# Kernel tuning notes

Hardware: AMD Instinct MI355X
Metric: run time of the kernel (lower is better)

Reference implementation:

```python
import jax, jax.numpy as jnp
import numpy as np

EMBED_DIM = 2048
N_HEADS = 16
N_KV_HEADS = 4
HEAD_DIM = EMBED_DIM // N_HEADS  # 128
B, T = 8, 512


def _rope_tables(seq, dim):
    # matches RoPE.__init__: freqs repeated twice along last dim
    inv_freq = 1.0 / (10000.0 ** (jnp.arange(0, dim, 2, dtype=jnp.float32) / dim))
    t = jnp.arange(seq, dtype=jnp.float32)
    freqs = jnp.outer(t, inv_freq)          # [T, dim/2]
    emb = jnp.concatenate([freqs, freqs], axis=-1)  # [T, dim]
    return jnp.cos(emb), jnp.sin(emb)


def _apply_rope(x, cos, sin):
    # x: [B, H, T, D]; rotate-half convention
    d2 = x.shape[-1] // 2
    x1, x2 = x[..., :d2], x[..., d2:]
    x_rot = jnp.concatenate([-x2, x1], axis=-1)
    return x * cos[None, None] + x_rot * sin[None, None]


def setup_inputs() -> dict:
    key = jax.random.key(0)
    k1, k2, k3, k4, k5 = jax.random.split(key, 5)
    x = jax.random.normal(k1, (B, T, EMBED_DIM), dtype=jnp.float32)
    s = 1.0 / np.sqrt(EMBED_DIM)
    # weights stored [in, out] for y = x @ W
    wq = jax.random.normal(k2, (EMBED_DIM, EMBED_DIM), dtype=jnp.float32) * s
    wk = jax.random.normal(k3, (EMBED_DIM, HEAD_DIM * N_KV_HEADS), dtype=jnp.float32) * s
    wv = jax.random.normal(k4, (EMBED_DIM, HEAD_DIM * N_KV_HEADS), dtype=jnp.float32) * s
    wo = jax.random.normal(k5, (EMBED_DIM, EMBED_DIM), dtype=jnp.float32) * s
    # causal mask: 1 where attendable, 0 -> masked to -inf
    mask = jnp.tril(jnp.ones((T, T), dtype=bool))[None, None]  # [1,1,T,T]
    return {"x": x, "wq": wq, "wk": wk, "wv": wv, "wo": wo, "mask": mask}


def reference(x, wq, wk, wv, wo, mask):
    Bx, Tx, C = x.shape
    rep = N_HEADS // N_KV_HEADS
    q = (x @ wq).reshape(Bx, Tx, N_HEADS, HEAD_DIM).transpose(0, 2, 1, 3)      # [B,H,T,D]
    k = (x @ wk).reshape(Bx, Tx, N_KV_HEADS, HEAD_DIM).transpose(0, 2, 1, 3)   # [B,Hk,T,D]
    v = (x @ wv).reshape(Bx, Tx, N_KV_HEADS, HEAD_DIM).transpose(0, 2, 1, 3)
    cos, sin = _rope_tables(Tx, HEAD_DIM)
    q = _apply_rope(q, cos, sin)
    k = _apply_rope(k, cos, sin)
    k = jnp.repeat(k, rep, axis=1)  # GQA expand -> [B,H,T,D]
    v = jnp.repeat(v, rep, axis=1)
    scale = HEAD_DIM ** -0.5
    attn = jnp.einsum('bhtd,bhsd->bhts', q, k) * scale  # [B,H,T,T]
    attn = jnp.where(mask, attn, -jnp.inf)
    attn = jax.nn.softmax(attn, axis=-1)
    out = jnp.einsum('bhts,bhsd->bhtd', attn, v)        # [B,H,T,D]
    out = out.transpose(0, 2, 1, 3).reshape(Bx, Tx, C)
    return out @ wo
```

## Files before the change

kernel.cpp:

```cpp
#include <hip/hip_runtime.h>
#include <hip/hip_bf16.h>
#include <stdint.h>


typedef __bf16 bf16x8 __attribute__((ext_vector_type(8)));
typedef float  f32x4  __attribute__((ext_vector_type(4)));
typedef float  f4     __attribute__((ext_vector_type(4)));
typedef unsigned short u16x8 __attribute__((ext_vector_type(8)));
typedef unsigned short u16x4 __attribute__((ext_vector_type(4)));
typedef unsigned short us;

template<int V> struct Ic { static constexpr int v = V; };

__device__ __forceinline__ float bf2f(us u) {
  unsigned int x = ((unsigned int)u) << 16;
  return __builtin_bit_cast(float, x);
}
__device__ __forceinline__ us f2bf(float f) {
  unsigned int x = __builtin_bit_cast(unsigned int, f);
  unsigned int r = x + 0x7fffu + ((x >> 16) & 1u);
  return (us)(r >> 16);
}

__device__ __forceinline__ void gload16(const void* gsrc, void* ldst) {
  auto g = (const __attribute__((address_space(1))) void*)gsrc;
  auto l = (__attribute__((address_space(3))) void*)ldst;
  __builtin_amdgcn_global_load_lds(g, l, 16, 0, 0);
}

#define BAR() __builtin_amdgcn_s_barrier()
#define LGK0() do { asm volatile("s_waitcnt lgkmcnt(0)" ::: "memory"); \
                    __builtin_amdgcn_sched_barrier(0); } while (0)
#define VM0() do { asm volatile("s_waitcnt vmcnt(0)" ::: "memory"); \
                   __builtin_amdgcn_sched_barrier(0); } while (0)


__global__ void convx_kernel(const float* __restrict__ x, us* __restrict__ xb) {
  size_t idx = (size_t)blockIdx.x * 256 + threadIdx.x;
  const f4* p = (const f4*)(x + idx * 8);
  f4 a = p[0], b = p[1];
  u16x8 o;
#pragma unroll
  for (int e = 0; e < 4; ++e) { o[e] = f2bf(a[e]); o[4 + e] = f2bf(b[e]); }
  *(u16x8*)(xb + idx * 8) = o;
}

__global__ __launch_bounds__(256) void wtrans_kernel(const float* __restrict__ src,
    us* __restrict__ dst, int N, int rowOff, int LD) {
  __shared__ float lds[64][65];
  const int n0 = blockIdx.x * 64, k0 = blockIdx.y * 64;
  const int c = threadIdx.x & 63, rq = threadIdx.x >> 6;
#pragma unroll
  for (int i = 0; i < 16; ++i) {
    int r = i * 4 + rq;
    lds[r][c] = src[(size_t)(k0 + r) * N + n0 + c];
  }
  __syncthreads();
#pragma unroll
  for (int i = 0; i < 16; ++i) {
    int nr = i * 4 + rq;
    dst[(size_t)(rowOff + n0 + nr) * LD + k0 + c] = f2bf(lds[c][nr]);
  }
}

__global__ void tables_kernel(float* __restrict__ ct, float* __restrict__ st) {
  int idx = blockIdx.x * 256 + threadIdx.x;
  int i = idx & 63, t = idx >> 6;
  float inv = exp2f(-(float)i * (13.287712379549449f / 64.0f));
  float ang = (float)t * inv;
  ct[idx] = cosf(ang);
  st[idx] = sinf(ang);
}

__global__ void rope_kernel(us* __restrict__ Qh, us* __restrict__ Kh,
                            const float* __restrict__ ct, const float* __restrict__ st) {
  int idx = blockIdx.x * 256 + threadIdx.x;
  int dq = idx & 15;
  int t = (idx >> 4) & 511;
  int slot = idx >> 13;
  bool isQ = slot < 128;
  us* rowp = isQ ? (Qh + ((size_t)slot * 512 + t) * 128)
                 : (Kh + ((size_t)(slot - 128) * 512 + t) * 128);
  int d0 = dq * 4;
  u16x4 x1 = *(const u16x4*)(rowp + d0);
  u16x4 x2 = *(const u16x4*)(rowp + 64 + d0);
  f4 c = *(const f4*)(ct + t * 64 + d0);
  f4 s = *(const f4*)(st + t * 64 + d0);
  float scale = isQ ? 0.08838834764831845f : 1.0f;
  u16x4 o1, o2;
#pragma unroll
  for (int e = 0; e < 4; ++e) {
    float a = bf2f(x1[e]), b = bf2f(x2[e]);
    o1[e] = f2bf((a * c[e] - b * s[e]) * scale);
    o2[e] = f2bf((b * c[e] + a * s[e]) * scale);
  }
  *(u16x4*)(rowp + d0) = o1;
  *(u16x4*)(rowp + 64 + d0) = o2;
}

__global__ __launch_bounds__(256) void vtrans_kernel(const us* __restrict__ Vh,
                                                     us* __restrict__ Vt) {
  __shared__ us lds[64][66];
  const int bid = blockIdx.x;
  const int bhk = bid >> 4;
  const int rem = bid & 15;
  const int tt = rem >> 1, dt = rem & 1;
  const us* src = Vh + (size_t)bhk * 512 * 128;
  us* dst = Vt + (size_t)bhk * 128 * 512;
  const int c = threadIdx.x & 63, rq = threadIdx.x >> 6;
#pragma unroll
  for (int i = 0; i < 16; ++i) {
    int r = i * 4 + rq;
    lds[r][c] = src[(size_t)(tt * 64 + r) * 128 + dt * 64 + c];
  }
  __syncthreads();
#pragma unroll
  for (int i = 0; i < 16; ++i) {
    int dr = i * 4 + rq;
    dst[(size_t)(dt * 64 + dr) * 512 + tt * 64 + c] = lds[c][dr];
  }
}

template<int BM, int BN, int MF, int NF, int GPT, int WN>
__device__ __forceinline__ void gemm8_core(const us* __restrict__ A,
    const us* __restrict__ Bt, int K, int m0, int n0, us* sm,
    f32x4 (&acc)[MF][NF]) {
  constexpr int MH = MF / 2, NH = NF / 2;
  constexpr int ACH = BM * 8, CH2 = (BM + BN) * 4;
  constexpr int BBASE = 2 * BM * 64;
  const int tid = threadIdx.x, lane = tid & 63, wid = tid >> 6;
  const int wm = wid / WN, wn = wid % WN;
  const int lr = lane & 15, lq = lane >> 4;
  const int NT2 = K >> 7;

  const f32x4 zz = {0.f, 0.f, 0.f, 0.f};
#pragma unroll
  for (int i = 0; i < MF; ++i)
#pragma unroll
    for (int j = 0; j < NF; ++j) acc[i][j] = zz;

  bf16x8 afr[MH][2], bfr[NH][2];

  auto stage_half = [&](int kt, int hf) {
    const int q = kt & 1;
#pragma unroll
    for (int i = 0; i < GPT; ++i) {
      int c = hf * CH2 + i * 512 + tid;
      bool isA = (c < ACH);
      int cc = isA ? c : c - ACH;
      int row = cc >> 3;
      int kcs = (cc & 7) ^ (row & 7);
      const us* src = (isA ? A + (size_t)(m0 + row) * K
                           : Bt + (size_t)(n0 + row) * K) + (kt << 6) + (kcs << 3);
      us* dst = sm + (isA ? q * BM * 64 + cc * 8 : BBASE + q * BN * 64 + cc * 8);
      gload16(src, dst);
    }
  };
  auto lda = [&](int q, int mq) {
#pragma unroll
    for (int f = 0; f < MH; ++f) {
      int R = wm * (MF * 16) + mq * (MH * 16) + f * 16 + lr;
      int base = (q * BM * 64 + R * 64) * 2;
      int sw = (R & 7) << 4;
#pragma unroll
      for (int ks = 0; ks < 2; ++ks)
        afr[f][ks] = *(const bf16x8*)((const char*)sm + base + ((ks * 64 + lq * 16) ^ sw));
    }
  };
  auto ldb = [&](int q, int nq) {
#pragma unroll
    for (int g = 0; g < NH; ++g) {
      int R = wn * (NF * 16) + nq * (NH * 16) + g * 16 + lr;
      int base = (BBASE + q * BN * 64 + R * 64) * 2;
      int sw = (R & 7) << 4;
#pragma unroll
      for (int ks = 0; ks < 2; ++ks)
        bfr[g][ks] = *(const bf16x8*)((const char*)sm + base + ((ks * 64 + lq * 16) ^ sw));
    }
  };
  auto mmac = [&](auto MQ, auto NQ) {
    constexpr int mq = decltype(MQ)::v, nq = decltype(NQ)::v;
    __builtin_amdgcn_s_setprio(1);
#pragma unroll
    for (int ks = 0; ks < 2; ++ks)
#pragma unroll
      for (int f = 0; f < MH; ++f)
#pragma unroll
        for (int g = 0; g < NH; ++g)
          acc[mq * MH + f][nq * NH + g] = __builtin_amdgcn_mfma_f32_16x16x32_bf16(
              afr[f][ks], bfr[g][ks], acc[mq * MH + f][nq * NH + g], 0, 0, 0);
    __builtin_amdgcn_s_setprio(0);
  };

  stage_half(0, 0); stage_half(0, 1);
  VM0(); BAR();

  for (int it = 0; it < NT2; ++it) {
    const int k0 = 2 * it;
    const bool pf = (it + 1 < NT2);
    lda(0, 0); ldb(0, 0);
    stage_half(k0 + 1, 0);
    BAR(); LGK0(); mmac(Ic<0>{}, Ic<0>{}); BAR();

    ldb(0, 1);
    stage_half(k0 + 1, 1);
    BAR(); LGK0(); mmac(Ic<0>{}, Ic<1>{}); BAR();

    lda(0, 1);
    BAR(); LGK0(); mmac(Ic<1>{}, Ic<1>{}); BAR();

    ldb(0, 0);
    BAR(); LGK0(); mmac(Ic<1>{}, Ic<0>{});
    VM0();
    BAR();
    lda(1, 0); ldb(1, 0);
    if (pf) stage_half(k0 + 2, 0);
    BAR(); LGK0(); mmac(Ic<0>{}, Ic<0>{}); BAR();

    ldb(1, 1);
    if (pf) stage_half(k0 + 2, 1);
    BAR(); LGK0(); mmac(Ic<0>{}, Ic<1>{}); BAR();

    lda(1, 1);
    BAR(); LGK0(); mmac(Ic<1>{}, Ic<1>{}); BAR();

    ldb(1, 0);
    BAR(); LGK0(); mmac(Ic<1>{}, Ic<0>{});
    VM0();
    BAR();
  }
}

__global__ __launch_bounds__(512, 2) void gemm_qkv8_kernel(const us* __restrict__ xb,
    const us* __restrict__ wcat, us* __restrict__ Qh, us* __restrict__ Kh,
    us* __restrict__ Vh) {
  __shared__ __align__(16) us sm[65536];
  const int bid = blockIdx.x;
  const int swz = (bid & 7) * 24 + (bid >> 3);
  const int m0 = (swz & 15) << 8, n0 = (swz >> 4) << 8;
  f32x4 acc[8][4];
  gemm8_core<256, 256, 8, 4, 4, 4>(xb, wcat, 2048, m0, n0, sm, acc);

  const int tid = threadIdx.x, lane = tid & 63, wid = tid >> 6;
  const int wm = wid >> 2, wn = wid & 3, lr = lane & 15, lq = lane >> 4;
#pragma unroll
  for (int f = 0; f < 8; ++f)
#pragma unroll
    for (int g = 0; g < 4; ++g) {
      int col = n0 + wn * 64 + g * 16 + lr;
#pragma unroll
      for (int r = 0; r < 4; ++r) {
        int row = m0 + wm * 128 + f * 16 + lq * 4 + r;
        int bb = row >> 9, t = row & 511;
        us val = f2bf(acc[f][g][r]);
        if (col < 2048) {
          Qh[((size_t)(bb * 16 + (col >> 7)) * 512 + t) * 128 + (col & 127)] = val;
        } else if (col < 2560) {
          int cc = col - 2048;
          Kh[((size_t)(bb * 4 + (cc >> 7)) * 512 + t) * 128 + (cc & 127)] = val;
        } else {
          int cc = col - 2560;
          Vh[((size_t)(bb * 4 + (cc >> 7)) * 512 + t) * 128 + (cc & 127)] = val;
        }
      }
    }
}

__global__ __launch_bounds__(512, 2) void gemm_out8_kernel(const us* __restrict__ Ob,
    const us* __restrict__ wot, float* __restrict__ out) {
  __shared__ __align__(16) us sm[49152];
  const int bid = blockIdx.x;
  const int swz = (bid & 7) * 32 + (bid >> 3);
  const int m0 = (swz & 15) << 8, n0 = (swz >> 4) << 7;
  f32x4 acc[4][4];
  gemm8_core<256, 128, 4, 4, 3, 2>(Ob, wot, 2048, m0, n0, sm, acc);

  const int tid = threadIdx.x, lane = tid & 63, wid = tid >> 6;
  const int wm = wid >> 1, wn = wid & 1, lr = lane & 15, lq = lane >> 4;
#pragma unroll
  for (int f = 0; f < 4; ++f)
#pragma unroll
    for (int g = 0; g < 4; ++g) {
      int col = n0 + wn * 64 + g * 16 + lr;
#pragma unroll
      for (int r = 0; r < 4; ++r) {
        int row = m0 + wm * 64 + f * 16 + lq * 4 + r;
        out[(size_t)row * 2048 + col] = acc[f][g][r];
      }
    }
}

__global__ __launch_bounds__(256) void attn_kernel(const us* __restrict__ Qh,
    const us* __restrict__ Kh, const us* __restrict__ Vt, us* __restrict__ Oh) {
  __shared__ __align__(16) us Ktile[64 * 128];
  __shared__ __align__(16) us Vtile[128 * 64];
  __shared__ __align__(16) us Plds[4 * 16 * 72];
  const int tid = threadIdx.x, lane = tid & 63, w = tid >> 6;
  const int lr = lane & 15, lq = lane >> 4;
  const int qb = blockIdx.x, bh = blockIdx.y;
  const int b = bh >> 4, h = bh & 15, kvh = h >> 2;
  const us* Kbh = Kh + (size_t)(b * 4 + kvh) * 512 * 128;
  const us* Vbh = Vt + (size_t)(b * 4 + kvh) * 128 * 512;

  const us* Qrow = Qh + ((size_t)bh * 512 + qb * 64 + w * 16 + lr) * 128;
  bf16x8 qf[4];
#pragma unroll
  for (int ks = 0; ks < 4; ++ks) qf[ks] = *(const bf16x8*)(Qrow + ks * 32 + (lq << 3));

  const f32x4 zz = {0.f, 0.f, 0.f, 0.f};
  f32x4 o[8];
#pragma unroll
  for (int i = 0; i < 8; ++i) o[i] = zz;
  float m[4], ll[4];
#pragma unroll
  for (int r = 0; r < 4; ++r) { m[r] = -1e30f; ll[r] = 0.f; }
  us* Pw = Plds + w * 16 * 72;

  for (int j = 0; j <= qb; ++j) {
    __syncthreads();
#pragma unroll
    for (int it = 0; it < 4; ++it) {
      int c = it * 256 + tid;
      int row = c >> 4, kc = c & 15;
      gload16(Kbh + (size_t)(j * 64 + row) * 128 + ((kc ^ (row & 7)) << 3),
              Ktile + (c << 3));
    }
#pragma unroll
    for (int it = 0; it < 4; ++it) {
      int c = it * 256 + tid;
      int row = c >> 3, tc = c & 7;
      gload16(Vbh + (size_t)row * 512 + j * 64 + ((tc ^ (row & 7)) << 3),
              Vtile + (c << 3));
    }
    __syncthreads();

    f32x4 s[4];
#pragma unroll
    for (int nb = 0; nb < 4; ++nb) s[nb] = zz;
#pragma unroll
    for (int ks = 0; ks < 4; ++ks) {
#pragma unroll
      for (int nb = 0; nb < 4; ++nb) {
        int row = nb * 16 + lr;
        bf16x8 kf = *(const bf16x8*)(Ktile + (row << 7) + (((ks * 4 + lq) ^ (row & 7)) << 3));
        s[nb] = __builtin_amdgcn_mfma_f32_16x16x32_bf16(qf[ks], kf, s[nb], 0, 0, 0);
      }
    }
    if (j == qb) {
#pragma unroll
      for (int nb = 0; nb < 4; ++nb)
#pragma unroll
        for (int r = 0; r < 4; ++r)
          if (nb * 16 + lr > w * 16 + lq * 4 + r) s[nb][r] = -1e30f;
    }

    float tm[4], alpha[4], rs[4];
#pragma unroll
    for (int r = 0; r < 4; ++r)
      tm[r] = fmaxf(fmaxf(s[0][r], s[1][r]), fmaxf(s[2][r], s[3][r]));
#pragma unroll
    for (int off = 1; off < 16; off <<= 1)
#pragma unroll
      for (int r = 0; r < 4; ++r)
        tm[r] = fmaxf(tm[r], __shfl_xor(tm[r], off, 64));
#pragma unroll
    for (int r = 0; r < 4; ++r) {
      float mn = fmaxf(m[r], tm[r]);
      alpha[r] = __expf(m[r] - mn);
      m[r] = mn;
    }
#pragma unroll
    for (int nb = 0; nb < 4; ++nb)
#pragma unroll
      for (int r = 0; r < 4; ++r)
        s[nb][r] = __expf(s[nb][r] - m[r]);
#pragma unroll
    for (int r = 0; r < 4; ++r)
      rs[r] = s[0][r] + s[1][r] + s[2][r] + s[3][r];
#pragma unroll
    for (int off = 1; off < 16; off <<= 1)
#pragma unroll
      for (int r = 0; r < 4; ++r)
        rs[r] += __shfl_xor(rs[r], off, 64);
#pragma unroll
    for (int r = 0; r < 4; ++r) ll[r] = ll[r] * alpha[r] + rs[r];
#pragma unroll
    for (int i = 0; i < 8; ++i)
#pragma unroll
      for (int r = 0; r < 4; ++r) o[i][r] *= alpha[r];

#pragma unroll
    for (int nb = 0; nb < 4; ++nb)
#pragma unroll
      for (int r = 0; r < 4; ++r)
        Pw[(lq * 4 + r) * 72 + nb * 16 + lr] = f2bf(s[nb][r]);

#pragma unroll
    for (int ks2 = 0; ks2 < 2; ++ks2) {
      bf16x8 pf = *(const bf16x8*)(Pw + lr * 72 + ks2 * 32 + (lq << 3));
#pragma unroll
      for (int nd = 0; nd < 8; ++nd) {
        int d = nd * 16 + lr;
        bf16x8 vf = *(const bf16x8*)(Vtile + (d << 6) + (((ks2 * 4 + lq) ^ (d & 7)) << 3));
        o[nd] = __builtin_amdgcn_mfma_f32_16x16x32_bf16(pf, vf, o[nd], 0, 0, 0);
      }
    }
  }

  float inv[4];
#pragma unroll
  for (int r = 0; r < 4; ++r) inv[r] = 1.0f / ll[r];
  const int rowb = b * 512 + qb * 64 + w * 16 + lq * 4;
  const int colb = h * 128 + lr;
#pragma unroll
  for (int nd = 0; nd < 8; ++nd)
#pragma unroll
    for (int r = 0; r < 4; ++r)
      Oh[(size_t)(rowb + r) * 2048 + colb + nd * 16] = f2bf(o[nd][r] * inv[r]);
}

extern "C" void kernel_launch(void* const* d_in, const int* in_sizes, int n_in,
                              void* d_out, int out_size, void* d_ws, size_t ws_size,
                              hipStream_t stream) {
  const float* x  = (const float*)d_in[0];
  const float* wq = (const float*)d_in[1];
  const float* wk = (const float*)d_in[2];
  const float* wv = (const float*)d_in[3];
  const float* wo = (const float*)d_in[4];
  float* out = (float*)d_out;
  char* ws = (char*)d_ws;

  us*    xb   = (us*)(ws);
  us*    wcat = (us*)(ws + 16777216);
  us*    wot  = (us*)(ws + 29360128);
  us*    Qh   = (us*)(ws + 37748736);
  us*    Kh   = (us*)(ws + 54525952);
  us*    Vh   = (us*)(ws + 58720256);
  us*    Vt   = (us*)(ws + 62914560);
  us*    Oh   = (us*)(ws + 67108864);
  float* ct   = (float*)(ws + 83886080);
  float* st   = (float*)(ws + 84017152);

  convx_kernel<<<4096, 256, 0, stream>>>(x, xb);
  wtrans_kernel<<<dim3(32, 32), 256, 0, stream>>>(wq, wcat, 2048, 0, 2048);
  wtrans_kernel<<<dim3(8, 32), 256, 0, stream>>>(wk, wcat, 512, 2048, 2048);
  wtrans_kernel<<<dim3(8, 32), 256, 0, stream>>>(wv, wcat, 512, 2560, 2048);
  wtrans_kernel<<<dim3(32, 32), 256, 0, stream>>>(wo, wot, 2048, 0, 2048);
  tables_kernel<<<128, 256, 0, stream>>>(ct, st);

  gemm_qkv8_kernel<<<192, 512, 0, stream>>>(xb, wcat, Qh, Kh, Vh);
  rope_kernel<<<5120, 256, 0, stream>>>(Qh, Kh, ct, st);
  vtrans_kernel<<<512, 256, 0, stream>>>(Vh, Vt);
  attn_kernel<<<dim3(8, 128), 256, 0, stream>>>(Qh, Kh, Vt, Oh);
  gemm_out8_kernel<<<256, 512, 0, stream>>>(Oh, wot, out);
}
```

Baseline: 184.0 us.

## Restructure GEMM pipeline to per-half-tile staging with partial vmcnt waits

Rewrites the shared GEMM core so each K-step of 64 is staged as four independent A/B half-tiles. Each quadrant MFMA phase waits only on the half-tiles it needs, using partial s_waitcnt vmcnt counts instead of full vmcnt(0) drains, so global-to-LDS loads overlap compute more finely. The out-projection warp layout changes from 4x2 to 2x4 waves, and the four weight-transpose launches are merged into one kernel to cut launch overhead. The vmcnt accounting depends on exact load counts per half and is fragile if the tile shapes change.

```diff
diff --git a/kernel.cpp b/kernel.cpp
--- a/kernel.cpp
+++ b/kernel.cpp
@@ -31,8 +31,15 @@
 #define BAR() __builtin_amdgcn_s_barrier()
 #define LGK0() do { asm volatile("s_waitcnt lgkmcnt(0)" ::: "memory"); \
                     __builtin_amdgcn_sched_barrier(0); } while (0)
-#define VM0() do { asm volatile("s_waitcnt vmcnt(0)" ::: "memory"); \
-                   __builtin_amdgcn_sched_barrier(0); } while (0)
+
+template<int N> __device__ __forceinline__ void VMW() {
+  if constexpr (N == 0)      asm volatile("s_waitcnt vmcnt(0)" ::: "memory");
+  else if constexpr (N == 2) asm volatile("s_waitcnt vmcnt(2)" ::: "memory");
+  else if constexpr (N == 3) asm volatile("s_waitcnt vmcnt(3)" ::: "memory");
+  else if constexpr (N == 4) asm volatile("s_waitcnt vmcnt(4)" ::: "memory");
+  else static_assert(N == 0 || N == 2 || N == 3 || N == 4, "unsupported vmcnt");
+  __builtin_amdgcn_sched_barrier(0);
+}
 
 
 __global__ void convx_kernel(const float* __restrict__ x, us* __restrict__ xb) {
@@ -45,10 +52,18 @@
   *(u16x8*)(xb + idx * 8) = o;
 }
 
-__global__ __launch_bounds__(256) void wtrans_kernel(const float* __restrict__ src,
-    us* __restrict__ dst, int N, int rowOff, int LD) {
+__global__ __launch_bounds__(256) void wtrans_all_kernel(
+    const float* __restrict__ wq, const float* __restrict__ wk,
+    const float* __restrict__ wv, const float* __restrict__ wo,
+    us* __restrict__ wcat, us* __restrict__ wot) {
   __shared__ float lds[64][65];
-  const int n0 = blockIdx.x * 64, k0 = blockIdx.y * 64;
+  int bx = blockIdx.x;
+  const float* src; us* dst; int N, rowOff, nb;
+  if (bx < 32)      { src = wq; dst = wcat; N = 2048; rowOff = 0;    nb = bx; }
+  else if (bx < 40) { src = wk; dst = wcat; N = 512;  rowOff = 2048; nb = bx - 32; }
+  else if (bx < 48) { src = wv; dst = wcat; N = 512;  rowOff = 2560; nb = bx - 40; }
+  else              { src = wo; dst = wot;  N = 2048; rowOff = 0;    nb = bx - 48; }
+  const int n0 = nb * 64, k0 = blockIdx.y * 64;
   const int c = threadIdx.x & 63, rq = threadIdx.x >> 6;
 #pragma unroll
   for (int i = 0; i < 16; ++i) {
@@ -59,7 +74,7 @@
 #pragma unroll
   for (int i = 0; i < 16; ++i) {
     int nr = i * 4 + rq;
-    dst[(size_t)(rowOff + n0 + nr) * LD + k0 + c] = f2bf(lds[c][nr]);
+    dst[(size_t)(rowOff + n0 + nr) * 2048 + k0 + c] = f2bf(lds[c][nr]);
   }
 }
 
@@ -121,17 +136,19 @@
   }
 }
 
-template<int BM, int BN, int MF, int NF, int GPT, int WN>
+template<int BM, int BN, int WM, int WN>
 __device__ __forceinline__ void gemm8_core(const us* __restrict__ A,
-    const us* __restrict__ Bt, int K, int m0, int n0, us* sm,
-    f32x4 (&acc)[MF][NF]) {
+    const us* __restrict__ Bt, const int K, const int m0, const int n0,
+    us* sm, f32x4 (&acc)[BM / (16 * WM)][BN / (16 * WN)]) {
+  constexpr int MF = BM / (16 * WM), NF = BN / (16 * WN);
   constexpr int MH = MF / 2, NH = NF / 2;
-  constexpr int ACH = BM * 8, CH2 = (BM + BN) * 4;
-  constexpr int BBASE = 2 * BM * 64;
+  constexpr int QM = MH * 16, QN = NH * 16;
+  constexpr int AHALF = (BM / 2) * 64, ABUF = BM * 64, ALDS = 2 * ABUF;
+  constexpr int BHALF = (BN / 2) * 64, BBUF = BN * 64;
+  constexpr int AL = BM / 128, BL = BN / 128;
   const int tid = threadIdx.x, lane = tid & 63, wid = tid >> 6;
   const int wm = wid / WN, wn = wid % WN;
   const int lr = lane & 15, lq = lane >> 4;
-  const int NT2 = K >> 7;
 
   const f32x4 zz = {0.f, 0.f, 0.f, 0.f};
 #pragma unroll
@@ -141,41 +158,48 @@
 
   bf16x8 afr[MH][2], bfr[NH][2];
 
-  auto stage_half = [&](int kt, int hf) {
-    const int q = kt & 1;
-#pragma unroll
-    for (int i = 0; i < GPT; ++i) {
-      int c = hf * CH2 + i * 512 + tid;
-      bool isA = (c < ACH);
-      int cc = isA ? c : c - ACH;
-      int row = cc >> 3;
-      int kcs = (cc & 7) ^ (row & 7);
-      const us* src = (isA ? A + (size_t)(m0 + row) * K
-                           : Bt + (size_t)(n0 + row) * K) + (kt << 6) + (kcs << 3);
-      us* dst = sm + (isA ? q * BM * 64 + cc * 8 : BBASE + q * BN * 64 + cc * 8);
-      gload16(src, dst);
+  auto stageA = [&](int kt, int qd, int h) {
+#pragma unroll
+    for (int i = 0; i < AL; ++i) {
+      int c = i * 512 + tid;
+      int lrow = c >> 3;
+      int grow = (lrow / QM) * (2 * QM) + h * QM + (lrow % QM);
+      int kcs = (c & 7) ^ (lrow & 7);
+      gload16(A + (size_t)(m0 + grow) * K + (kt << 6) + (kcs << 3),
+              sm + qd * ABUF + h * AHALF + c * 8);
     }
   };
-  auto lda = [&](int q, int mq) {
+  auto stageB = [&](int kt, int qd, int h) {
+#pragma unroll
+    for (int i = 0; i < BL; ++i) {
+      int c = i * 512 + tid;
+      int lrow = c >> 3;
+      int grow = (lrow / QN) * (2 * QN) + h * QN + (lrow % QN);
+      int kcs = (c & 7) ^ (lrow & 7);
+      gload16(Bt + (size_t)(n0 + grow) * K + (kt << 6) + (kcs << 3),
+              sm + ALDS + qd * BBUF + h * BHALF + c * 8);
+    }
+  };
+  auto lda = [&](int q, int h) {
 #pragma unroll
     for (int f = 0; f < MH; ++f) {
-      int R = wm * (MF * 16) + mq * (MH * 16) + f * 16 + lr;
-      int base = (q * BM * 64 + R * 64) * 2;
+      int R = wm * QM + f * 16 + lr;
+      const char* base = (const char*)(sm + q * ABUF + h * AHALF + R * 64);
       int sw = (R & 7) << 4;
 #pragma unroll
       for (int ks = 0; ks < 2; ++ks)
-        afr[f][ks] = *(const bf16x8*)((const char*)sm + base + ((ks * 64 + lq * 16) ^ sw));
+        afr[f][ks] = *(const bf16x8*)(base + ((ks * 64 + lq * 16) ^ sw));
     }
   };
-  auto ldb = [&](int q, int nq) {
+  auto ldb = [&](int q, int h) {
 #pragma unroll
     for (int g = 0; g < NH; ++g) {
-      int R = wn * (NF * 16) + nq * (NH * 16) + g * 16 + lr;
-      int base = (BBASE + q * BN * 64 + R * 64) * 2;
+      int R = wn * QN + g * 16 + lr;
+      const char* base = (const char*)(sm + ALDS + q * BBUF + h * BHALF + R * 64);
       int sw = (R & 7) << 4;
 #pragma unroll
       for (int ks = 0; ks < 2; ++ks)
-        bfr[g][ks] = *(const bf16x8*)((const char*)sm + base + ((ks * 64 + lq * 16) ^ sw));
+        bfr[g][ks] = *(const bf16x8*)(base + ((ks * 64 + lq * 16) ^ sw));
     }
   };
   auto mmac = [&](auto MQ, auto NQ) {
@@ -192,41 +216,31 @@
     __builtin_amdgcn_s_setprio(0);
   };
 
-  stage_half(0, 0); stage_half(0, 1);
-  VM0(); BAR();
-
-  for (int it = 0; it < NT2; ++it) {
-    const int k0 = 2 * it;
-    const bool pf = (it + 1 < NT2);
-    lda(0, 0); ldb(0, 0);
-    stage_half(k0 + 1, 0);
-    BAR(); LGK0(); mmac(Ic<0>{}, Ic<0>{}); BAR();
-
-    ldb(0, 1);
-    stage_half(k0 + 1, 1);
-    BAR(); LGK0(); mmac(Ic<0>{}, Ic<1>{}); BAR();
-
-    lda(0, 1);
-    BAR(); LGK0(); mmac(Ic<1>{}, Ic<1>{}); BAR();
-
-    ldb(0, 0);
+  stageA(0, 0, 0); stageB(0, 0, 0); stageB(0, 0, 1); stageA(0, 0, 1);
+  VMW<AL + BL>(); BAR();
+
+  const int NT = K >> 6;
+  for (int kt = 0; kt < NT; ++kt) {
+    const int q = kt & 1, qn = q ^ 1;
+    const bool pf = (kt + 1 < NT);
+    lda(q, 0); ldb(q, 0);
+    if (pf) stageA(kt + 1, qn, 0);
+    BAR(); LGK0(); mmac(Ic<0>{}, Ic<0>{});
+    if (pf) VMW<2 * AL>(); else VMW<AL>();
+    BAR();
+    ldb(q, 1);
+    if (pf) stageB(kt + 1, qn, 0);
+    BAR(); LGK0(); mmac(Ic<0>{}, Ic<1>{});
+    if (pf) VMW<AL + BL>(); else VMW<0>();
+    BAR();
+    lda(q, 1);
+    if (pf) stageB(kt + 1, qn, 1);
+    BAR(); LGK0(); mmac(Ic<1>{}, Ic<1>{});
+    BAR();
+    ldb(q, 0);
+    if (pf) stageA(kt + 1, qn, 1);
     BAR(); LGK0(); mmac(Ic<1>{}, Ic<0>{});
-    VM0();
-    BAR();
-    lda(1, 0); ldb(1, 0);
-    if (pf) stage_half(k0 + 2, 0);
-    BAR(); LGK0(); mmac(Ic<0>{}, Ic<0>{}); BAR();
-
-    ldb(1, 1);
-    if (pf) stage_half(k0 + 2, 1);
-    BAR(); LGK0(); mmac(Ic<0>{}, Ic<1>{}); BAR();
-
-    lda(1, 1);
-    BAR(); LGK0(); mmac(Ic<1>{}, Ic<1>{}); BAR();
-
-    ldb(1, 0);
-    BAR(); LGK0(); mmac(Ic<1>{}, Ic<0>{});
-    VM0();
+    if (pf) VMW<AL + BL>();
     BAR();
   }
 }
@@ -239,7 +253,7 @@
   const int swz = (bid & 7) * 24 + (bid >> 3);
   const int m0 = (swz & 15) << 8, n0 = (swz >> 4) << 8;
   f32x4 acc[8][4];
-  gemm8_core<256, 256, 8, 4, 4, 4>(xb, wcat, 2048, m0, n0, sm, acc);
+  gemm8_core<256, 256, 2, 4>(xb, wcat, 2048, m0, n0, sm, acc);
 
   const int tid = threadIdx.x, lane = tid & 63, wid = tid >> 6;
   const int wm = wid >> 2, wn = wid & 3, lr = lane & 15, lq = lane >> 4;
@@ -272,19 +286,19 @@
   const int bid = blockIdx.x;
   const int swz = (bid & 7) * 32 + (bid >> 3);
   const int m0 = (swz & 15) << 8, n0 = (swz >> 4) << 7;
-  f32x4 acc[4][4];
-  gemm8_core<256, 128, 4, 4, 3, 2>(Ob, wot, 2048, m0, n0, sm, acc);
+  f32x4 acc[8][2];
+  gemm8_core<256, 128, 2, 4>(Ob, wot, 2048, m0, n0, sm, acc);
 
   const int tid = threadIdx.x, lane = tid & 63, wid = tid >> 6;
-  const int wm = wid >> 1, wn = wid & 1, lr = lane & 15, lq = lane >> 4;
-#pragma unroll
-  for (int f = 0; f < 4; ++f)
-#pragma unroll
-    for (int g = 0; g < 4; ++g) {
-      int col = n0 + wn * 64 + g * 16 + lr;
+  const int wm = wid >> 2, wn = wid & 3, lr = lane & 15, lq = lane >> 4;
+#pragma unroll
+  for (int f = 0; f < 8; ++f)
+#pragma unroll
+    for (int g = 0; g < 2; ++g) {
+      int col = n0 + wn * 32 + g * 16 + lr;
 #pragma unroll
       for (int r = 0; r < 4; ++r) {
-        int row = m0 + wm * 64 + f * 16 + lq * 4 + r;
+        int row = m0 + wm * 128 + f * 16 + lq * 4 + r;
         out[(size_t)row * 2048 + col] = acc[f][g][r];
       }
     }
@@ -442,10 +456,7 @@
   float* st   = (float*)(ws + 84017152);
 
   convx_kernel<<<4096, 256, 0, stream>>>(x, xb);
-  wtrans_kernel<<<dim3(32, 32), 256, 0, stream>>>(wq, wcat, 2048, 0, 2048);
-  wtrans_kernel<<<dim3(8, 32), 256, 0, stream>>>(wk, wcat, 512, 2048, 2048);
-  wtrans_kernel<<<dim3(8, 32), 256, 0, stream>>>(wv, wcat, 512, 2560, 2048);
-  wtrans_kernel<<<dim3(32, 32), 256, 0, stream>>>(wo, wot, 2048, 0, 2048);
+  wtrans_all_kernel<<<dim3(80, 32), 256, 0, stream>>>(wq, wk, wv, wo, wcat, wot);
   tables_kernel<<<128, 256, 0, stream>>>(ct, st);
 
   gemm_qkv8_kernel<<<192, 512, 0, stream>>>(xb, wcat, Qh, Kh, Vh);
```

Result: faster. 175.0 us (-4.9%).
